# Kernel tuning notes

Hardware: AMD Instinct MI355X
Metric: run time of the kernel (lower is better)

## Reference

```python
import jax, jax.numpy as jnp
import numpy as np

B, T, D, H = 2, 2048, 2048, 16
HD = D // H
EPS = 1e-8
NEG = -1e9


def setup_inputs() -> dict:
    key = jax.random.key(0)
    ks = jax.random.split(key, 6)
    x = jax.random.normal(ks[0], (B, T, D), dtype=jnp.float32)
    # additive causal mask, broadcast over [B, H, T, T]
    causal = jnp.tril(jnp.ones((T, T), dtype=bool))
    attn_mask = jnp.where(causal, 0.0, NEG).astype(jnp.float32)[None, None]
    s = 1.0 / np.sqrt(D)
    w_norm = jnp.ones((D,), dtype=jnp.float32)
    wq = jax.random.normal(ks[1], (D, D), dtype=jnp.float32) * s
    wk = jax.random.normal(ks[2], (D, D), dtype=jnp.float32) * s
    wv = jax.random.normal(ks[3], (D, D), dtype=jnp.float32) * s
    wo = jax.random.normal(ks[4], (D, D), dtype=jnp.float32) * s
    return {"x": x, "attn_mask": attn_mask, "w_norm": w_norm,
            "wq": wq, "wk": wk, "wv": wv, "wo": wo}


def _rmsnorm(x, w):
    # norm = ||x||_2 * D^-0.5 ; out = w * x / (norm + eps)  (eps outside, as in source)
    norm = jnp.sqrt(jnp.sum(x * x, axis=-1, keepdims=True)) * (x.shape[-1] ** -0.5)
    return w * x / (norm + EPS)


def reference(x, attn_mask, w_norm, wq, wk, wv, wo):
    b, t, d = x.shape
    xn = _rmsnorm(x, w_norm)
    # Linear (no bias): y = x @ W^T ; split into heads -> [B, H, T, HD]
    def proj(w):
        return jnp.einsum('btd,ed->bte', xn, w).reshape(b, t, H, HD).transpose(0, 2, 1, 3)
    q, k, v = proj(wq), proj(wk), proj(wv)
    scale = HD ** -0.5
    w_scores = jnp.einsum('bhqd,bhkd->bhqk', q, k) * scale + attn_mask
    p = jax.nn.softmax(w_scores, axis=-1)
    out = jnp.einsum('bhqk,bhkd->bhqd', p, v)
    out = out.transpose(0, 2, 1, 3).reshape(b, t, d)
    return jnp.einsum('btd,ed->bte', out, wo)
```

## Files before the change

kernel.cpp:

```cpp
#include <hip/hip_runtime.h>
#include <stdint.h>

#define TT 2048
#define DD 2048
#define NHH 16
#define HDD 128
#define BTT 4096

typedef __attribute__((ext_vector_type(8))) short bf16x8;
typedef __attribute__((ext_vector_type(4))) float f32x4;

#define MF(a, b, c) __builtin_amdgcn_mfma_f32_16x16x32_bf16(a, b, c, 0, 0, 0)

__device__ __forceinline__ unsigned short f2bf(float f) {
    union { float f; uint32_t u; } v; v.f = f;
    uint32_t u = v.u;
    u += 0x7fffu + ((u >> 16) & 1u);
    return (unsigned short)(u >> 16);
}

__device__ __forceinline__ void gld16(const unsigned short* g, unsigned short* l) {
    __builtin_amdgcn_global_load_lds(
        (const __attribute__((address_space(1))) unsigned int*)g,
        (__attribute__((address_space(3))) unsigned int*)l, 16, 0, 0);
}

__global__ __launch_bounds__(256) void convert_w(const float* __restrict__ wq,
                                                 const float* __restrict__ wk,
                                                 const float* __restrict__ wv,
                                                 const float* __restrict__ wo,
                                                 unsigned short* __restrict__ out) {
    size_t gid = (size_t)blockIdx.x * 256 + threadIdx.x;
    size_t base = gid * 8;
    int which = (int)(base >> 22);
    const float* src = which == 0 ? wq : which == 1 ? wk : which == 2 ? wv : wo;
    size_t off = base & 4194303u;
    float4 a = ((const float4*)(src + off))[0];
    float4 b = ((const float4*)(src + off))[1];
    union { unsigned short us[8]; uint4 v; } pk;
    pk.us[0] = f2bf(a.x); pk.us[1] = f2bf(a.y); pk.us[2] = f2bf(a.z); pk.us[3] = f2bf(a.w);
    pk.us[4] = f2bf(b.x); pk.us[5] = f2bf(b.y); pk.us[6] = f2bf(b.z); pk.us[7] = f2bf(b.w);
    *(uint4*)(out + base) = pk.v;
}

__global__ __launch_bounds__(256) void rmsnorm_k(const float* __restrict__ x,
                                                 const float* __restrict__ w,
                                                 unsigned short* __restrict__ xn) {
    const int row = blockIdx.x;
    const int tid = threadIdx.x;
    const float* xr = x + (size_t)row * DD;
    float4 a = ((const float4*)xr)[tid * 2];
    float4 b = ((const float4*)xr)[tid * 2 + 1];
    float ss = a.x*a.x + a.y*a.y + a.z*a.z + a.w*a.w
             + b.x*b.x + b.y*b.y + b.z*b.z + b.w*b.w;
    #pragma unroll
    for (int m = 1; m < 64; m <<= 1) ss += __shfl_xor(ss, m, 64);
    __shared__ float wss[4];
    if ((tid & 63) == 0) wss[tid >> 6] = ss;
    __syncthreads();
    float total = wss[0] + wss[1] + wss[2] + wss[3];
    float norm = sqrtf(total) * 0.022097086912079612f;
    float inv = 1.0f / (norm + 1e-8f);
    float4 wa = ((const float4*)w)[tid * 2];
    float4 wb = ((const float4*)w)[tid * 2 + 1];
    union { unsigned short us[8]; uint4 v; } pk;
    pk.us[0] = f2bf(wa.x * a.x * inv); pk.us[1] = f2bf(wa.y * a.y * inv);
    pk.us[2] = f2bf(wa.z * a.z * inv); pk.us[3] = f2bf(wa.w * a.w * inv);
    pk.us[4] = f2bf(wb.x * b.x * inv); pk.us[5] = f2bf(wb.y * b.y * inv);
    pk.us[6] = f2bf(wb.z * b.z * inv); pk.us[7] = f2bf(wb.w * b.w * inv);
    ((uint4*)(xn + (size_t)row * DD))[tid] = pk.v;
}

__device__ __forceinline__ void gemm128x256_core(const unsigned short* __restrict__ Ag,
                                                 const unsigned short* __restrict__ Bg,
                                                 unsigned short* lds, f32x4 acc[4][4]) {
    const int tid = threadIdx.x;
    const int wave = tid >> 6, lane = tid & 63;
    const int wm = wave >> 2, wn = wave & 3;
    const int l15 = lane & 15, lq = lane >> 4, r7 = l15 & 7;
    const int gr = lane >> 3;
    const size_t goff = (size_t)gr * DD + (size_t)(((lane & 7) ^ gr) * 8);
    const int xk0 = (lq ^ r7) * 8;
    const int xk1 = ((4 + lq) ^ r7) * 8;
    const int aro = (wm * 64 + l15) * 64;
    const int bro = 8192 + (wn * 64 + l15) * 64;
    const int swA = wave * 16;
    const int swB = wave * 32;

    #pragma unroll
    for (int c = 0; c < 2; c++)
        gld16(Ag + (size_t)(swA + c * 8) * DD + goff, lds + (swA + c * 8) * 64);
    #pragma unroll
    for (int c = 0; c < 4; c++)
        gld16(Bg + (size_t)(swB + c * 8) * DD + goff, lds + 8192 + (swB + c * 8) * 64);
    asm volatile("s_waitcnt vmcnt(0)" ::: "memory");
    __builtin_amdgcn_sched_barrier(0);
    __builtin_amdgcn_s_barrier();

    for (int kt = 0; kt < DD / 64; kt++) {
        const int cur = (kt & 1) ? 24576 : 0;
        const int nxt = 24576 - cur;
        const bool hn = (kt + 1 < DD / 64);
        const int kn = (kt + 1) * 64;
        const unsigned short* ac = lds + cur + aro;
        const unsigned short* bc = lds + cur + bro;
        bf16x8 afA[2][2], afB[2][2], bA[2][2], bB[2][2];

        #pragma unroll
        for (int m = 0; m < 2; m++) {
            afA[m][0] = *(const bf16x8*)(ac + m * 1024 + xk0);
            afA[m][1] = *(const bf16x8*)(ac + m * 1024 + xk1);
            afB[m][0] = *(const bf16x8*)(ac + (2 + m) * 1024 + xk0);
            afB[m][1] = *(const bf16x8*)(ac + (2 + m) * 1024 + xk1);
        }
        #pragma unroll
        for (int n = 0; n < 2; n++) {
            bA[n][0] = *(const bf16x8*)(bc + n * 1024 + xk0);
            bA[n][1] = *(const bf16x8*)(bc + n * 1024 + xk1);
        }
        if (hn) {
            #pragma unroll
            for (int c = 0; c < 2; c++)
                gld16(Ag + (size_t)(swA + c * 8) * DD + kn + goff,
                      lds + nxt + (swA + c * 8) * 64);
            #pragma unroll
            for (int c = 0; c < 4; c++)
                gld16(Bg + (size_t)(swB + c * 8) * DD + kn + goff,
                      lds + nxt + 8192 + (swB + c * 8) * 64);
        }
        __builtin_amdgcn_s_barrier();
        asm volatile("s_waitcnt lgkmcnt(0)" ::: "memory");
        __builtin_amdgcn_sched_barrier(0);
        __builtin_amdgcn_s_setprio(1);
        #pragma unroll
        for (int m = 0; m < 2; m++)
            #pragma unroll
            for (int n = 0; n < 2; n++) {
                acc[m][n]     = MF(afA[m][0], bA[n][0], acc[m][n]);
                acc[m][n]     = MF(afA[m][1], bA[n][1], acc[m][n]);
                acc[2 + m][n] = MF(afB[m][0], bA[n][0], acc[2 + m][n]);
                acc[2 + m][n] = MF(afB[m][1], bA[n][1], acc[2 + m][n]);
            }
        __builtin_amdgcn_s_setprio(0);
        __builtin_amdgcn_s_barrier();

        #pragma unroll
        for (int n = 0; n < 2; n++) {
            bB[n][0] = *(const bf16x8*)(bc + (2 + n) * 1024 + xk0);
            bB[n][1] = *(const bf16x8*)(bc + (2 + n) * 1024 + xk1);
        }
        __builtin_amdgcn_s_barrier();
        asm volatile("s_waitcnt lgkmcnt(0)" ::: "memory");
        __builtin_amdgcn_sched_barrier(0);
        __builtin_amdgcn_s_setprio(1);
        #pragma unroll
        for (int m = 0; m < 2; m++)
            #pragma unroll
            for (int n = 0; n < 2; n++) {
                acc[m][2 + n]     = MF(afA[m][0], bB[n][0], acc[m][2 + n]);
                acc[m][2 + n]     = MF(afA[m][1], bB[n][1], acc[m][2 + n]);
                acc[2 + m][2 + n] = MF(afB[m][0], bB[n][0], acc[2 + m][2 + n]);
                acc[2 + m][2 + n] = MF(afB[m][1], bB[n][1], acc[2 + m][2 + n]);
            }
        __builtin_amdgcn_s_setprio(0);
        asm volatile("s_waitcnt vmcnt(0)" ::: "memory");
        __builtin_amdgcn_sched_barrier(0);
        __builtin_amdgcn_s_barrier();
    }
}

__global__ __launch_bounds__(512, 2) void gemm_qkv(const unsigned short* __restrict__ A,
                                                   const unsigned short* __restrict__ W3,
                                                   unsigned short* __restrict__ O3) {
    __shared__ __align__(16) unsigned short lds[49152];
    const int orig = blockIdx.y * 32 + blockIdx.x;
    const int id = (orig & 7) * 96 + (orig >> 3);
    const int which = id >> 8;
    const int rem = id & 255;
    const int bn = rem >> 5, bm = rem & 31;
    const unsigned short* Bw = W3 + (size_t)which * DD * DD;
    unsigned short* C = O3 + (size_t)which * BTT * DD;
    const int m0 = bm * 128, n0 = bn * 256;
    const f32x4 zf = {0.f, 0.f, 0.f, 0.f};
    f32x4 acc[4][4];
    #pragma unroll
    for (int m = 0; m < 4; m++)
        #pragma unroll
        for (int n = 0; n < 4; n++) acc[m][n] = zf;
    gemm128x256_core(A + (size_t)m0 * DD, Bw + (size_t)n0 * DD, lds, acc);
    const int wave = threadIdx.x >> 6, lane = threadIdx.x & 63;
    const int wm = wave >> 2, wn = wave & 3;
    const int l15 = lane & 15, lq = lane >> 4;
    #pragma unroll
    for (int m = 0; m < 4; m++) {
        const int row = m0 + wm * 64 + m * 16 + lq * 4;
        #pragma unroll
        for (int n = 0; n < 4; n++) {
            const int col = n0 + wn * 64 + n * 16 + l15;
            #pragma unroll
            for (int r = 0; r < 4; r++)
                C[(size_t)(row + r) * DD + col] = f2bf(acc[m][n][r]);
        }
    }
}

__global__ __launch_bounds__(512, 2) void gemm_out(const unsigned short* __restrict__ A,
                                                   const unsigned short* __restrict__ Bw,
                                                   float* __restrict__ C) {
    __shared__ __align__(16) unsigned short lds[49152];
    const int orig = blockIdx.y * 32 + blockIdx.x;
    const int id = (orig & 7) * 32 + (orig >> 3);
    const int bn = id >> 5, bm = id & 31;
    const int m0 = bm * 128, n0 = bn * 256;
    const f32x4 zf = {0.f, 0.f, 0.f, 0.f};
    f32x4 acc[4][4];
    #pragma unroll
    for (int m = 0; m < 4; m++)
        #pragma unroll
        for (int n = 0; n < 4; n++) acc[m][n] = zf;
    gemm128x256_core(A + (size_t)m0 * DD, Bw + (size_t)n0 * DD, lds, acc);
    const int wave = threadIdx.x >> 6, lane = threadIdx.x & 63;
    const int wm = wave >> 2, wn = wave & 3;
    const int l15 = lane & 15, lq = lane >> 4;
    #pragma unroll
    for (int m = 0; m < 4; m++) {
        const int row = m0 + wm * 64 + m * 16 + lq * 4;
        #pragma unroll
        for (int n = 0; n < 4; n++) {
            const int col = n0 + wn * 64 + n * 16 + l15;
            #pragma unroll
            for (int r = 0; r < 4; r++)
                C[(size_t)(row + r) * DD + col] = acc[m][n][r];
        }
    }
}

__global__ __launch_bounds__(256) void attn_fused(const unsigned short* __restrict__ q,
                                                  const unsigned short* __restrict__ k,
                                                  const unsigned short* __restrict__ v,
                                                  unsigned short* __restrict__ o) {
    constexpr int LKK = 136;
    constexpr int LPP = 72;
    __shared__ __align__(16) unsigned short Ks[2][64 * LKK];
    __shared__ __align__(16) unsigned short Vts[128 * 64];
    __shared__ __align__(16) unsigned short Ps[4 * 16 * LPP];
    const int h = blockIdx.y, b = blockIdx.z;
    const int tid = threadIdx.x, wave = tid >> 6, lane = tid & 63;
    const int l15 = lane & 15, lq = lane >> 4;
    const size_t rowbase = (size_t)b * TT;
    const int hcol = h * HDD;
    const float scale = 0.08838834764831845f;
    unsigned short* Pw = Ps + wave * 16 * LPP;
    const f32x4 zf = {0.f, 0.f, 0.f, 0.f};

    uint4 kr0, kr1, kr2, kr3, vr0, vr1, vr2, vr3;
    const int sidx = tid * 8;
    const int srr = sidx >> 7;
    const int sc  = sidx & 127;
    const int swz = ((sc >> 3) & 7) << 3;
    const int srs0 = (srr +  0) ^ swz;
    const int srs1 = (srr + 16) ^ swz;
    const int srs2 = (srr + 32) ^ swz;
    const int srs3 = (srr + 48) ^ swz;

    for (int half = 0; half < 2; half++) {
        const int qj = (half == 0) ? blockIdx.x : 31 - blockIdx.x;
        const int qt0 = qj * 64;
        bf16x8 aq[4];
        {
            const unsigned short* qrp = q + (rowbase + qt0 + wave * 16 + l15) * DD + hcol;
            #pragma unroll
            for (int kk = 0; kk < 4; kk++)
                aq[kk] = *(const bf16x8*)(qrp + kk * 32 + lq * 8);
        }
        f32x4 acc_o[8];
        #pragma unroll
        for (int jh = 0; jh < 8; jh++) acc_o[jh] = zf;
        float m_i[4], l_i[4];
        #pragma unroll
        for (int r = 0; r < 4; r++) { m_i[r] = -1e30f; l_i[r] = 0.f; }
        const int qp0 = qt0 + wave * 16 + lq * 4;
        const int nkt = qj + 1;

        __syncthreads();
        {
            const unsigned short* kg = k + rowbase * DD + hcol;
            const unsigned short* vg = v + rowbase * DD + hcol;
            kr0 = *(const uint4*)(kg + (size_t)(srr +  0) * DD + sc);
            kr1 = *(const uint4*)(kg + (size_t)(srr + 16) * DD + sc);
            kr2 = *(const uint4*)(kg + (size_t)(srr + 32) * DD + sc);
            kr3 = *(const uint4*)(kg + (size_t)(srr + 48) * DD + sc);
            vr0 = *(const uint4*)(vg + (size_t)(srr +  0) * DD + sc);
            vr1 = *(const uint4*)(vg + (size_t)(srr + 16) * DD + sc);
            vr2 = *(const uint4*)(vg + (size_t)(srr + 32) * DD + sc);
            vr3 = *(const uint4*)(vg + (size_t)(srr + 48) * DD + sc);
            unsigned short* ksb = &Ks[0][0];
            *(uint4*)(ksb + (srr +  0) * LKK + sc) = kr0;
            *(uint4*)(ksb + (srr + 16) * LKK + sc) = kr1;
            *(uint4*)(ksb + (srr + 32) * LKK + sc) = kr2;
            *(uint4*)(ksb + (srr + 48) * LKK + sc) = kr3;
            if (nkt > 1) {
                const unsigned short* kg1 = k + (rowbase + 64) * DD + hcol;
                kr0 = *(const uint4*)(kg1 + (size_t)(srr +  0) * DD + sc);
                kr1 = *(const uint4*)(kg1 + (size_t)(srr + 16) * DD + sc);
                kr2 = *(const uint4*)(kg1 + (size_t)(srr + 32) * DD + sc);
                kr3 = *(const uint4*)(kg1 + (size_t)(srr + 48) * DD + sc);
            }
        }

        for (int kt = 0; kt < nkt; kt++) {
            const int cur = kt & 1;
            __syncthreads();
            {
                const unsigned short* d0 = (const unsigned short*)&vr0;
                const unsigned short* d1 = (const unsigned short*)&vr1;
                const unsigned short* d2 = (const unsigned short*)&vr2;
                const unsigned short* d3 = (const unsigned short*)&vr3;
                #pragma unroll
                for (int jj = 0; jj < 8; jj++) {
                    Vts[(sc + jj) * 64 + srs0] = d0[jj];
                    Vts[(sc + jj) * 64 + srs1] = d1[jj];
                    Vts[(sc + jj) * 64 + srs2] = d2[jj];
                    Vts[(sc + jj) * 64 + srs3] = d3[jj];
                }
            }
            if (kt + 1 < nkt) {
                unsigned short* ksb = &Ks[cur ^ 1][0];
                *(uint4*)(ksb + (srr +  0) * LKK + sc) = kr0;
                *(uint4*)(ksb + (srr + 16) * LKK + sc) = kr1;
                *(uint4*)(ksb + (srr + 32) * LKK + sc) = kr2;
                *(uint4*)(ksb + (srr + 48) * LKK + sc) = kr3;
            }
            if (kt + 2 < nkt) {
                const unsigned short* kg = k + (rowbase + (kt + 2) * 64) * DD + hcol;
                kr0 = *(const uint4*)(kg + (size_t)(srr +  0) * DD + sc);
                kr1 = *(const uint4*)(kg + (size_t)(srr + 16) * DD + sc);
                kr2 = *(const uint4*)(kg + (size_t)(srr + 32) * DD + sc);
                kr3 = *(const uint4*)(kg + (size_t)(srr + 48) * DD + sc);
            }
            if (kt + 1 < nkt) {
                const unsigned short* vg = v + (rowbase + (kt + 1) * 64) * DD + hcol;
                vr0 = *(const uint4*)(vg + (size_t)(srr +  0) * DD + sc);
                vr1 = *(const uint4*)(vg + (size_t)(srr + 16) * DD + sc);
                vr2 = *(const uint4*)(vg + (size_t)(srr + 32) * DD + sc);
                vr3 = *(const uint4*)(vg + (size_t)(srr + 48) * DD + sc);
            }
            const unsigned short* ksc = &Ks[cur][0];
            f32x4 accs[4];
            #pragma unroll
            for (int j = 0; j < 4; j++) accs[j] = zf;
            __builtin_amdgcn_s_setprio(1);
            #pragma unroll
            for (int j = 0; j < 4; j++)
                #pragma unroll
                for (int kk = 0; kk < 4; kk++) {
                    bf16x8 bk = *(const bf16x8*)(&ksc[(j * 16 + l15) * LKK + kk * 32 + lq * 8]);
                    accs[j] = MF(aq[kk], bk, accs[j]);
                }
            __builtin_amdgcn_s_setprio(0);
            const int kbase = kt * 64;
            float rowmax[4] = {-1e30f, -1e30f, -1e30f, -1e30f};
            #pragma unroll
            for (int j = 0; j < 4; j++) {
                const int kp = kbase + j * 16 + l15;
                #pragma unroll
                for (int r = 0; r < 4; r++) {
                    float s = accs[j][r] * scale;
                    s = (kp > qp0 + r) ? -1e30f : s;
                    accs[j][r] = s;
                    rowmax[r] = fmaxf(rowmax[r], s);
                }
            }
            #pragma unroll
            for (int r = 0; r < 4; r++) {
                float mx = rowmax[r];
                mx = fmaxf(mx, __shfl_xor(mx, 1, 64));
                mx = fmaxf(mx, __shfl_xor(mx, 2, 64));
                mx = fmaxf(mx, __shfl_xor(mx, 4, 64));
                mx = fmaxf(mx, __shfl_xor(mx, 8, 64));
                float m_new = fmaxf(m_i[r], mx);
                float al = __expf(m_i[r] - m_new);
                m_i[r] = m_new;
                l_i[r] *= al;
                #pragma unroll
                for (int jh = 0; jh < 8; jh++) acc_o[jh][r] *= al;
            }
            float rowsum[4] = {0.f, 0.f, 0.f, 0.f};
            #pragma unroll
            for (int j = 0; j < 4; j++)
                #pragma unroll
                for (int r = 0; r < 4; r++) {
                    float p = __expf(accs[j][r] - m_i[r]);
                    rowsum[r] += p;
                    Pw[(lq * 4 + r) * LPP + j * 16 + l15] = f2bf(p);
                }
            #pragma unroll
            for (int r = 0; r < 4; r++) {
                float s = rowsum[r];
                s += __shfl_xor(s, 1, 64);
                s += __shfl_xor(s, 2, 64);
                s += __shfl_xor(s, 4, 64);
                s += __shfl_xor(s, 8, 64);
                l_i[r] += s;
            }
            __syncthreads();
            bf16x8 ap[2];
            #pragma unroll
            for (int kk = 0; kk < 2; kk++)
                ap[kk] = *(const bf16x8*)(&Pw[l15 * LPP + kk * 32 + lq * 8]);
            __builtin_amdgcn_s_setprio(1);
            #pragma unroll
            for (int jh = 0; jh < 8; jh++) {
                const int hd = jh * 16 + l15;
                const int vswz = ((hd >> 3) & 7) << 3;
                #pragma unroll
                for (int kk = 0; kk < 2; kk++) {
                    bf16x8 bv = *(const bf16x8*)(&Vts[hd * 64 + ((kk * 32 + lq * 8) ^ vswz)]);
                    acc_o[jh] = MF(ap[kk], bv, acc_o[jh]);
                }
            }
            __builtin_amdgcn_s_setprio(0);
        }
        #pragma unroll
        for (int jh = 0; jh < 8; jh++) {
            const int col = hcol + jh * 16 + l15;
            #pragma unroll
            for (int r = 0; r < 4; r++)
                o[(rowbase + qp0 + r) * DD + col] = f2bf(acc_o[jh][r] * (1.0f / l_i[r]));
        }
    }
}

extern "C" void kernel_launch(void* const* d_in, const int* in_sizes, int n_in,
                              void* d_out, int out_size, void* d_ws, size_t ws_size,
                              hipStream_t stream) {
    const float* x      = (const float*)d_in[0];
    const float* w_norm = (const float*)d_in[2];
    const float* wq     = (const float*)d_in[3];
    const float* wk     = (const float*)d_in[4];
    const float* wv     = (const float*)d_in[5];
    const float* wo     = (const float*)d_in[6];

    unsigned short* wbf = (unsigned short*)d_ws;
    unsigned short* xn  = wbf + (size_t)4 * DD * DD;
    unsigned short* qb  = xn + (size_t)BTT * DD;
    unsigned short* kb  = qb + (size_t)BTT * DD;
    unsigned short* vb  = kb + (size_t)BTT * DD;
    unsigned short* ab  = vb + (size_t)BTT * DD;

    convert_w<<<8192, 256, 0, stream>>>(wq, wk, wv, wo, wbf);
    rmsnorm_k<<<BTT, 256, 0, stream>>>(x, w_norm, xn);
    dim3 gqkv(32, 24);
    gemm_qkv<<<gqkv, 512, 0, stream>>>(xn, wbf, qb);
    dim3 gattn(16, NHH, 2);
    attn_fused<<<gattn, 256, 0, stream>>>(qb, kb, vb, ab);
    dim3 gout(32, 8);
    gemm_out<<<gout, 512, 0, stream>>>(ab, wbf + (size_t)3 * DD * DD, (float*)d_out);
}
```

Before: 429.7 us.

## Load K tiles via direct global-to-LDS with XOR swizzle, pack V transposed stores

```diff
diff --git a/kernel.cpp b/kernel.cpp
--- a/kernel.cpp
+++ b/kernel.cpp
@@ -239,9 +239,8 @@
                                                   const unsigned short* __restrict__ k,
                                                   const unsigned short* __restrict__ v,
                                                   unsigned short* __restrict__ o) {
-    constexpr int LKK = 136;
     constexpr int LPP = 72;
-    __shared__ __align__(16) unsigned short Ks[2][64 * LKK];
+    __shared__ __align__(16) unsigned short Ks[2][64 * 128];
     __shared__ __align__(16) unsigned short Vts[128 * 64];
     __shared__ __align__(16) unsigned short Ps[4 * 16 * LPP];
     const int h = blockIdx.y, b = blockIdx.z;
@@ -253,15 +252,14 @@
     unsigned short* Pw = Ps + wave * 16 * LPP;
     const f32x4 zf = {0.f, 0.f, 0.f, 0.f};
 
-    uint4 kr0, kr1, kr2, kr3, vr0, vr1, vr2, vr3;
-    const int sidx = tid * 8;
-    const int srr = sidx >> 7;
-    const int sc  = sidx & 127;
-    const int swz = ((sc >> 3) & 7) << 3;
-    const int srs0 = (srr +  0) ^ swz;
-    const int srs1 = (srr + 16) ^ swz;
-    const int srs2 = (srr + 32) ^ swz;
-    const int srs3 = (srr + 48) ^ swz;
+    uint4 vr0, vr1, vr2, vr3;
+    const int pr = tid >> 3;
+    const int hc = (tid & 7) * 16;
+    const int vsw0 = (2 * pr) ^ (((hc >> 3) & 7) << 3);
+    const int vsw1 = (2 * pr) ^ ((((hc + 8) >> 3) & 7) << 3);
+
+    const int klrow = lane >> 4;
+    const int klch  = lane & 15;
 
     for (int half = 0; half < 2; half++) {
         const int qj = (half == 0) ? blockIdx.x : 31 - blockIdx.x;
@@ -286,64 +284,51 @@
         {
             const unsigned short* kg = k + rowbase * DD + hcol;
             const unsigned short* vg = v + rowbase * DD + hcol;
-            kr0 = *(const uint4*)(kg + (size_t)(srr +  0) * DD + sc);
-            kr1 = *(const uint4*)(kg + (size_t)(srr + 16) * DD + sc);
-            kr2 = *(const uint4*)(kg + (size_t)(srr + 32) * DD + sc);
-            kr3 = *(const uint4*)(kg + (size_t)(srr + 48) * DD + sc);
-            vr0 = *(const uint4*)(vg + (size_t)(srr +  0) * DD + sc);
-            vr1 = *(const uint4*)(vg + (size_t)(srr + 16) * DD + sc);
-            vr2 = *(const uint4*)(vg + (size_t)(srr + 32) * DD + sc);
-            vr3 = *(const uint4*)(vg + (size_t)(srr + 48) * DD + sc);
-            unsigned short* ksb = &Ks[0][0];
-            *(uint4*)(ksb + (srr +  0) * LKK + sc) = kr0;
-            *(uint4*)(ksb + (srr + 16) * LKK + sc) = kr1;
-            *(uint4*)(ksb + (srr + 32) * LKK + sc) = kr2;
-            *(uint4*)(ksb + (srr + 48) * LKK + sc) = kr3;
-            if (nkt > 1) {
-                const unsigned short* kg1 = k + (rowbase + 64) * DD + hcol;
-                kr0 = *(const uint4*)(kg1 + (size_t)(srr +  0) * DD + sc);
-                kr1 = *(const uint4*)(kg1 + (size_t)(srr + 16) * DD + sc);
-                kr2 = *(const uint4*)(kg1 + (size_t)(srr + 32) * DD + sc);
-                kr3 = *(const uint4*)(kg1 + (size_t)(srr + 48) * DD + sc);
-            }
+            #pragma unroll
+            for (int i = 0; i < 4; i++) {
+                const int r0 = wave * 16 + i * 4;
+                const int row = r0 + klrow;
+                const int gch = klch ^ (row & 7);
+                gld16(kg + (size_t)row * DD + gch * 8, &Ks[0][r0 * 128]);
+            }
+            vr0 = *(const uint4*)(vg + (size_t)(2 * pr) * DD + hc);
+            vr1 = *(const uint4*)(vg + (size_t)(2 * pr) * DD + hc + 8);
+            vr2 = *(const uint4*)(vg + (size_t)(2 * pr + 1) * DD + hc);
+            vr3 = *(const uint4*)(vg + (size_t)(2 * pr + 1) * DD + hc + 8);
         }
 
         for (int kt = 0; kt < nkt; kt++) {
             const int cur = kt & 1;
             __syncthreads();
+            if (kt + 1 < nkt) {
+                const unsigned short* kg = k + (rowbase + (kt + 1) * 64) * DD + hcol;
+                #pragma unroll
+                for (int i = 0; i < 4; i++) {
+                    const int r0 = wave * 16 + i * 4;
+                    const int row = r0 + klrow;
+                    const int gch = klch ^ (row & 7);
+                    gld16(kg + (size_t)row * DD + gch * 8, &Ks[cur ^ 1][r0 * 128]);
+                }
+            }
             {
-                const unsigned short* d0 = (const unsigned short*)&vr0;
-                const unsigned short* d1 = (const unsigned short*)&vr1;
-                const unsigned short* d2 = (const unsigned short*)&vr2;
-                const unsigned short* d3 = (const unsigned short*)&vr3;
+                const unsigned short* s0 = (const unsigned short*)&vr0;
+                const unsigned short* s1 = (const unsigned short*)&vr1;
+                const unsigned short* s2 = (const unsigned short*)&vr2;
+                const unsigned short* s3 = (const unsigned short*)&vr3;
                 #pragma unroll
                 for (int jj = 0; jj < 8; jj++) {
-                    Vts[(sc + jj) * 64 + srs0] = d0[jj];
-                    Vts[(sc + jj) * 64 + srs1] = d1[jj];
-                    Vts[(sc + jj) * 64 + srs2] = d2[jj];
-                    Vts[(sc + jj) * 64 + srs3] = d3[jj];
-                }
-            }
-            if (kt + 1 < nkt) {
-                unsigned short* ksb = &Ks[cur ^ 1][0];
-                *(uint4*)(ksb + (srr +  0) * LKK + sc) = kr0;
-                *(uint4*)(ksb + (srr + 16) * LKK + sc) = kr1;
-                *(uint4*)(ksb + (srr + 32) * LKK + sc) = kr2;
-                *(uint4*)(ksb + (srr + 48) * LKK + sc) = kr3;
-            }
-            if (kt + 2 < nkt) {
-                const unsigned short* kg = k + (rowbase + (kt + 2) * 64) * DD + hcol;
-                kr0 = *(const uint4*)(kg + (size_t)(srr +  0) * DD + sc);
-                kr1 = *(const uint4*)(kg + (size_t)(srr + 16) * DD + sc);
-                kr2 = *(const uint4*)(kg + (size_t)(srr + 32) * DD + sc);
-                kr3 = *(const uint4*)(kg + (size_t)(srr + 48) * DD + sc);
+                    *(uint32_t*)(&Vts[(hc + jj) * 64 + vsw0]) =
+                        (uint32_t)s0[jj] | ((uint32_t)s2[jj] << 16);
+                    *(uint32_t*)(&Vts[(hc + 8 + jj) * 64 + vsw1]) =
+                        (uint32_t)s1[jj] | ((uint32_t)s3[jj] << 16);
+                }
             }
             if (kt + 1 < nkt) {
                 const unsigned short* vg = v + (rowbase + (kt + 1) * 64) * DD + hcol;
-                vr0 = *(const uint4*)(vg + (size_t)(srr +  0) * DD + sc);
-                vr1 = *(const uint4*)(vg + (size_t)(srr + 16) * DD + sc);
-                vr2 = *(const uint4*)(vg + (size_t)(srr + 32) * DD + sc);
-                vr3 = *(const uint4*)(vg + (size_t)(srr + 48) * DD + sc);
+                vr0 = *(const uint4*)(vg + (size_t)(2 * pr) * DD + hc);
+                vr1 = *(const uint4*)(vg + (size_t)(2 * pr) * DD + hc + 8);
+                vr2 = *(const uint4*)(vg + (size_t)(2 * pr + 1) * DD + hc);
+                vr3 = *(const uint4*)(vg + (size_t)(2 * pr + 1) * DD + hc + 8);
             }
             const unsigned short* ksc = &Ks[cur][0];
             f32x4 accs[4];
@@ -354,7 +339,8 @@
             for (int j = 0; j < 4; j++)
                 #pragma unroll
                 for (int kk = 0; kk < 4; kk++) {
-                    bf16x8 bk = *(const bf16x8*)(&ksc[(j * 16 + l15) * LKK + kk * 32 + lq * 8]);
+                    bf16x8 bk = *(const bf16x8*)(&ksc[(j * 16 + l15) * 128 +
+                                                      (((kk * 4 + lq) ^ (l15 & 7)) * 8)]);
                     accs[j] = MF(aq[kk], bk, accs[j]);
                 }
             __builtin_amdgcn_s_setprio(0);
```

Result: no change. 426.8 us (-0.7%).
